# Kernel optimization log

Measured on AMD Instinct MI355X. Metric: run time of the kernel, lower is better.

## Reference

```python
import jax, jax.numpy as jnp
import numpy as np

B, T_ENC, VOCAB, HID = 256, 128, 1024, 1024
NUM_CLASSES = VOCAB - 1   # think_end_token
MAX_THINK = 16
N_OUT = T_ENC - 3


def setup_inputs() -> dict:
    key = jax.random.key(0)
    ks = jax.random.split(key, 8)
    s = 1.0 / np.sqrt(HID)
    x = jax.random.normal(ks[0], (B, T_ENC, VOCAB), jnp.float32)
    lengths = jax.random.randint(ks[1], (B,), 1, T_ENC + 1)  # valid lengths >= 1
    W_ih = jax.random.uniform(ks[2], (4 * HID, VOCAB), jnp.float32, -s, s)
    W_hh = jax.random.uniform(ks[3], (4 * HID, HID), jnp.float32, -s, s)
    b_ih = jax.random.uniform(ks[4], (4 * HID,), jnp.float32, -s, s)
    b_hh = jax.random.uniform(ks[5], (4 * HID,), jnp.float32, -s, s)
    W_fc = jax.random.uniform(ks[6], (VOCAB, HID), jnp.float32, -s, s)
    b_fc = jax.random.uniform(ks[7], (VOCAB,), jnp.float32, -s, s)
    return {"x": x, "W_ih": W_ih, "W_hh": W_hh, "b_ih": b_ih, "b_hh": b_hh,
            "W_fc": W_fc, "b_fc": b_fc, "lengths": lengths, "N": N_OUT}


def _lstm_cell(x_t, h, c, W_ih, W_hh, b):
    # torch gate order: i, f, g, o
    gates = x_t @ W_ih.T + h @ W_hh.T + b
    i, f, g, o = jnp.split(gates, 4, axis=-1)
    c_new = jax.nn.sigmoid(f) * c + jax.nn.sigmoid(i) * jnp.tanh(g)
    h_new = jax.nn.sigmoid(o) * jnp.tanh(c_new)
    return h_new, c_new


def reference(x, W_ih, W_hh, b_ih, b_hh, W_fc, b_fc, lengths, N):
    b = b_ih + b_hh
    Bsz = x.shape[0]
    h0 = jnp.zeros((Bsz, HID), x.dtype)
    c0 = jnp.zeros((Bsz, HID), x.dtype)

    # --- encoder: packed LSTM == masked scan, state frozen past each length ---
    def enc_step(carry, xt_t):
        h, c = carry
        xt, t = xt_t
        h_new, c_new = _lstm_cell(xt, h, c, W_ih, W_hh, b)
        m = (t < lengths)[:, None]
        return (jnp.where(m, h_new, h), jnp.where(m, c_new, c)), None

    (h, c), _ = jax.lax.scan(
        enc_step, (h0, c0),
        (jnp.transpose(x, (1, 0, 2)), jnp.arange(x.shape[1])))

    dec_in = x[jnp.arange(Bsz), lengths - 1, :]  # [B, VOCAB]
    T_dec = MAX_THINK + N  # while-loop terminates within this many steps
    fo0 = jnp.zeros((Bsz, N, VOCAB), x.dtype)
    key0 = jax.random.key(42)
    bidx = jnp.arange(Bsz)

    def dec_step(carry, t):
        h, c, cur, fo, think_steps, out_steps, is_think = carry
        outputting = (~is_think) & (out_steps < N)
        h, c = _lstm_cell(cur, h, c, W_ih, W_hh, b)
        logits = h @ W_fc.T + b_fc  # [B, VOCAB]
        # gumbel_softmax(tau=1, hard=True) with straight-through estimator
        gnoise = jax.random.gumbel(jax.random.fold_in(key0, t), logits.shape, logits.dtype)
        y_soft = jax.nn.softmax(logits + gnoise, axis=-1)
        y_hard = jax.nn.one_hot(jnp.argmax(y_soft, axis=-1), VOCAB, dtype=logits.dtype)
        one_hot_out = y_hard + y_soft - jax.lax.stop_gradient(y_soft)
        # masked scatter of logits into final_outputs at current output step
        step_idx = jnp.minimum(out_steps, N - 1)
        old = fo[bidx, step_idx]
        fo = fo.at[bidx, step_idx].set(jnp.where(outputting[:, None], logits, old))
        out_steps = out_steps + outputting.astype(out_steps.dtype)
        think_steps = think_steps + is_think.astype(think_steps.dtype)
        pred = jnp.argmax(one_hot_out, axis=-1)
        just_finished = is_think & ((pred == NUM_CLASSES) | (think_steps >= MAX_THINK))
        # original code: if any sample is thinking, next_input = logits for ALL
        nxt = jnp.where(jnp.any(is_think), logits, one_hot_out)
        is_think = is_think & (~just_finished)
        return (h, c, nxt, fo, think_steps, out_steps, is_think), None

    init = (h, c, dec_in, fo0,
            jnp.zeros(Bsz, jnp.int32), jnp.zeros(Bsz, jnp.int32),
            jnp.ones(Bsz, bool))
    (h, c, cur, fo, think_steps, out_steps, is_think), _ = jax.lax.scan(
        dec_step, init, jnp.arange(T_dec))
    return fo[:, :, :-1], think_steps
```

## Files before the change

kernel.cpp:

```cpp
#include <hip/hip_runtime.h>
#include <stdint.h>

#define HID 1024
#define NGATE 4096
#define BATCH 256
#define TENC 128
#define VOCAB 1024
#define NOUT 125
#define TDEC 141
#define MAXTHINK 16
#define STOPCLS 1023

typedef __attribute__((ext_vector_type(8))) short short8;
typedef __attribute__((ext_vector_type(4))) float f32x4;

#define WPLE ((size_t)NGATE*1024)
#define VPLE ((size_t)VOCAB*1024)
#define MFMA_B __builtin_amdgcn_mfma_f32_16x16x32_bf16

#define I_CLAIM 0
#define I_FLAGS 64
#define I_GEN   4224
#define I_ANY   4288
#define I_PRED  4608

#define LBAR() do { asm volatile("s_waitcnt lgkmcnt(0)" ::: "memory"); \
                    __builtin_amdgcn_s_barrier(); } while(0)

__device__ __forceinline__ uint32_t rotl32(uint32_t v, int r){ return (v<<r)|(v>>(32-r)); }

__device__ __forceinline__ void tf2x32(uint32_t k0, uint32_t k1, uint32_t x0, uint32_t x1,
                                       uint32_t& o0, uint32_t& o1)
{
  uint32_t k2 = k0 ^ k1 ^ 0x1BD11BDAu;
  x0 += k0; x1 += k1;
#define R4(a,b,cc,d) x0+=x1;x1=rotl32(x1,a);x1^=x0; x0+=x1;x1=rotl32(x1,b);x1^=x0; \
                     x0+=x1;x1=rotl32(x1,cc);x1^=x0; x0+=x1;x1=rotl32(x1,d);x1^=x0;
  R4(13,15,26,6)  x0+=k1; x1+=k2+1u;
  R4(17,29,16,24) x0+=k2; x1+=k0+2u;
  R4(13,15,26,6)  x0+=k0; x1+=k1+3u;
  R4(17,29,16,24) x0+=k1; x1+=k2+4u;
  R4(13,15,26,6)  x0+=k2; x1+=k0+5u;
#undef R4
  o0 = x0; o1 = x1;
}

__device__ __forceinline__ uint32_t jax_bits(uint32_t fk0, uint32_t fk1, uint32_t i)
{
  uint32_t o0, o1;
  tf2x32(fk0, fk1, 0u, i, o0, o1);
  return o0 ^ o1;
}

__device__ __forceinline__ float sigm(float x){ return 0.5f + 0.5f*tanhf(0.5f*x); }

__device__ __forceinline__ ushort bf16rn(float v){
  uint32_t u = __float_as_uint(v);
  uint32_t r = (u + 0x7fffu + ((u>>16)&1u)) >> 16;
  return (ushort)r;
}
__device__ __forceinline__ float bf16tof(ushort s){ return __uint_as_float(((uint32_t)s)<<16); }

typedef unsigned long long __attribute__((address_space(1))) gu64_t;
typedef int                __attribute__((address_space(1))) gi32_t;
typedef unsigned short     __attribute__((address_space(1))) gu16_t;

__device__ __forceinline__ uint64_t cld8(const ushort* p){
  return __hip_atomic_load((const gu64_t*)(uintptr_t)p, __ATOMIC_RELAXED, __HIP_MEMORY_SCOPE_AGENT);
}
__device__ __forceinline__ void cst8(ushort* p, uint64_t v){
  __hip_atomic_store((gu64_t*)(uintptr_t)p, v, __ATOMIC_RELAXED, __HIP_MEMORY_SCOPE_AGENT);
}
__device__ __forceinline__ float cld4f(const float* p){
  int v = __hip_atomic_load((const gi32_t*)(uintptr_t)p, __ATOMIC_RELAXED, __HIP_MEMORY_SCOPE_AGENT);
  return __int_as_float(v);
}
__device__ __forceinline__ void cst4f(float* p, float x){
  __hip_atomic_store((gi32_t*)(uintptr_t)p, __float_as_int(x), __ATOMIC_RELAXED, __HIP_MEMORY_SCOPE_AGENT);
}
__device__ __forceinline__ int cld4i(const int* p){
  return __hip_atomic_load((const gi32_t*)(uintptr_t)p, __ATOMIC_RELAXED, __HIP_MEMORY_SCOPE_AGENT);
}
__device__ __forceinline__ void cst4i(int* p, int v){
  __hip_atomic_store((gi32_t*)(uintptr_t)p, v, __ATOMIC_RELAXED, __HIP_MEMORY_SCOPE_AGENT);
}
__device__ __forceinline__ ushort cld2(const ushort* p){
  return __hip_atomic_load((const gu16_t*)(uintptr_t)p, __ATOMIC_RELAXED, __HIP_MEMORY_SCOPE_AGENT);
}
__device__ __forceinline__ void cst2(ushort* p, ushort v){
  __hip_atomic_store((gu16_t*)(uintptr_t)p, v, __ATOMIC_RELAXED, __HIP_MEMORY_SCOPE_AGENT);
}

typedef ushort GatesLds[2][3][32][40];
typedef ushort LdsXA[3][256][40];

__device__ __forceinline__ void gbar(int* flags, int* gen, int e, int rk, int tid)
{
  __syncthreads();
  if (tid == 0)
    __hip_atomic_store((gi32_t*)(uintptr_t)&flags[rk*16], e, __ATOMIC_RELAXED, __HIP_MEMORY_SCOPE_AGENT);
  if (rk == 0){
    if (tid < 256){
      while (cld4i(&flags[tid*16]) < e)
        __builtin_amdgcn_s_sleep(1);
    }
    __syncthreads();
    if (tid == 0)
      __hip_atomic_store((gi32_t*)(uintptr_t)gen, e, __ATOMIC_RELAXED, __HIP_MEMORY_SCOPE_AGENT);
  } else if (tid == 0){
    while (cld4i(gen) < e)
      __builtin_amdgcn_s_sleep(1);
  }
  __syncthreads();
}

__global__ __launch_bounds__(256) void prep_kernel(
    const float* __restrict__ b_ih, const float* __restrict__ b_hh,
    const float* __restrict__ x, const int* __restrict__ lengths,
    float* __restrict__ bsum, int* __restrict__ ints,
    ushort* __restrict__ h3i, ushort* __restrict__ cur3i,
    ushort* __restrict__ h3p0, ushort* __restrict__ curp0)
{
  int idx = blockIdx.x*256 + threadIdx.x;
  if (idx < NGATE) bsum[idx] = b_ih[idx] + b_hh[idx];
  if (idx < 8)   ints[I_CLAIM + idx] = 0;
  if (idx < 256) ints[I_FLAGS + idx*16] = 0;
  if (idx == 0)  ints[I_GEN] = 0;
  if (idx < TDEC+1) ints[I_ANY + idx] = (idx==0) ? 1 : 0;
  *(unsigned long long*)(h3i + (size_t)idx*4) = 0ull;
  h3p0[idx] = 0;
  int b = idx >> 10, k = idx & (HID-1);
  int L = lengths[b];
  float v = x[((size_t)b*TENC + (size_t)(L-1))*HID + k];
  ushort p0 = bf16rn(v); v -= bf16tof(p0);
  ushort p1 = bf16rn(v); v -= bf16tof(p1);
  ushort p2 = bf16rn(v);
  *(unsigned long long*)(cur3i + (size_t)idx*4) =
      (uint64_t)p0 | ((uint64_t)p1<<16) | ((uint64_t)p2<<32);
  curp0[idx] = p0;
}

__global__ __launch_bounds__(256) void splitw_kernel(
    const float* __restrict__ W, ushort* __restrict__ Wf, int N)
{
  int idx = blockIdx.x*256 + threadIdx.x;
  int n = idx >> 7, kc = idx & 127;
  float v[8];
  *(float4*)&v[0] = *(const float4*)(W + (size_t)n*1024 + kc*8);
  *(float4*)&v[4] = *(const float4*)(W + (size_t)n*1024 + kc*8 + 4);
  size_t base = ((size_t)(n>>4)*128 + kc)*128 + (n&15)*8;
  #pragma unroll
  for (int p=0;p<3;p++){
    ushort o[8];
    #pragma unroll
    for (int e=0;e<8;e++){ ushort pp = bf16rn(v[e]); v[e] -= bf16tof(pp); o[e] = pp; }
    *(uint4*)(Wf + (size_t)p*N*1024 + base) = *(uint4*)o;
  }
}


__device__ void xgemm_do(const float* __restrict__ x, const ushort* __restrict__ wih,
                         float* __restrict__ xg_x, int tc, int xcc, int rank,
                         char* xa_mem, int tid)
{
  LdsXA& xa = *reinterpret_cast<LdsXA*>(xa_mem);
  int lane = tid & 63, w = tid >> 6;
  int fr = lane & 15, q = lane >> 4;
  int tt = rank >> 2, g = rank & 3;
  int srow = tid >> 1, half = (tid & 1) * 16;
  const float* xrow = x + ((size_t)srow*TENC + (tc*8 + tt))*HID;
  size_t off = ((size_t)(g*64 + xcc*8 + w)*128 + q)*128 + fr*8;

#define LOADX(dst, kc) { \
  int kcl = ((kc) < 32) ? (kc) : 0; \
  _Pragma("unroll") for (int i=0;i<4;i++) \
    *(float4*)&dst[i*4] = *(const float4*)(xrow + kcl*32 + half + i*4); }

#define SPLITSTORE(xv) { \
  _Pragma("unroll") for (int p=0;p<3;p++){ \
    ushort o[16]; \
    _Pragma("unroll") for (int e=0;e<16;e++){ ushort pp = bf16rn(xv[e]); xv[e] -= bf16tof(pp); o[e] = pp; } \
    *(uint4*)&xa[p][srow][half]   = *(uint4*)&o[0]; \
    *(uint4*)&xa[p][srow][half+8] = *(uint4*)&o[8]; } }

#define XLOADB(dst, kc) { \
  int kcl = ((kc) < 32) ? (kc) : 0; \
  _Pragma("unroll") for (int p=0;p<3;p++) \
    dst[p] = *(const short8*)(wih + (size_t)p*WPLE + off + (size_t)kcl*512); }

#define XMFMA(bq) { \
  _Pragma("unroll") for (int mf=0; mf<16; mf++){ \
    short8 af[3]; \
    _Pragma("unroll") for (int p=0;p<3;p++) af[p] = *(const short8*)&xa[p][mf*16+fr][q*8]; \
    acc[mf] = MFMA_B(af[2], bq[0], acc[mf], 0,0,0); \
    acc[mf] = MFMA_B(af[1], bq[1], acc[mf], 0,0,0); \
    acc[mf] = MFMA_B(af[0], bq[2], acc[mf], 0,0,0); \
    acc[mf] = MFMA_B(af[1], bq[0], acc[mf], 0,0,0); \
    acc[mf] = MFMA_B(af[0], bq[1], acc[mf], 0,0,0); \
    acc[mf] = MFMA_B(af[0], bq[0], acc[mf], 0,0,0); } }

  f32x4 acc[16] = {};
  float xv0[16], xv1[16];
  short8 bq0[3], bq1[3];
  LOADX(xv0, 0); XLOADB(bq0, 0);
  for (int kc = 0; kc < 32; kc += 2){
    LBAR();
    SPLITSTORE(xv0);
    LBAR();
    LOADX(xv1, kc+1); XLOADB(bq1, kc+1);
    XMFMA(bq0);
    LBAR();
    SPLITSTORE(xv1);
    LBAR();
    LOADX(xv0, kc+2); XLOADB(bq0, kc+2);
    XMFMA(bq1);
  }
#undef LOADX
#undef SPLITSTORE
#undef XLOADB
#undef XMFMA
  #pragma unroll
  for (int mf=0; mf<16; mf++)
    #pragma unroll
    for (int r=0;r<4;r++)
      cst4f(xg_x + (size_t)(tt*256 + mf*16 + q*4 + r)*512 + g*128 + w*16 + fr, acc[mf][r]);
}

template<int PL, int MODE>
__device__ void gates_do(
    const ushort* __restrict__ A0i, const ushort* __restrict__ A1i,
    const ushort* __restrict__ A0c, const ushort* __restrict__ A1c,
    const ushort* __restrict__ Wih, const ushort* __restrict__ Whh,
    const float* __restrict__ Wihf, const int* __restrict__ pred,
    const float* __restrict__ xg_x,
    int t, const int* len2, const float (*bs2)[4],
    float* creg, ushort* __restrict__ h3newi, ushort* __restrict__ h3p0new,
    GatesLds& As, char* ep_mem,
    int xcc, int bb, int kg, int tid)
{
  constexpr int KT = (MODE==1) ? 64 : 32;
  float (*ep)[32][33] = reinterpret_cast<float(*)[32][33]>(ep_mem);
  int lane = tid & 63, w = tid >> 6;
  int fr = lane & 15, q = lane >> 4;
  int arow = tid >> 4, apos = tid & 15;
  int bf = w & 1, kf = (w>>1) & 1, gh = w >> 2;

  size_t off[2];
  #pragma unroll
  for (int g2=0; g2<2; g2++)
    off[g2] = ((size_t)((2*gh+g2)*64 + xcc*8 + kg*2 + kf)*128 + q)*128 + fr*8;

  f32x4 acc[2] = {};

#define LOADSA(sv, kc) { \
  int kcl = ((kc) < KT) ? (kc) : 0; \
  int kl = kcl & 31; \
  if constexpr (PL==3){ \
    const ushort* ai = (MODE==1 && kcl < 32) ? A0i : A1i; \
    _Pragma("unroll") for (int j=0;j<2;j++) \
      sv[j] = cld8(ai + ((size_t)(bb + arow)*1024 + kl*32 + apos*2 + j)*4); \
  } else { \
    const ushort* ac = (MODE==1 && kcl < 32) ? A0c : A1c; \
    sv[0] = (uint64_t)(uint)cld4i((const int*)(ac + (size_t)(bb + arow)*1024 + kl*32 + apos*2)); \
  } }

#define STAGE(buf, sv) { \
  if constexpr (PL==3){ \
    _Pragma("unroll") for (int p=0;p<3;p++){ \
      uint lo = (uint)((sv[0] >> (16*p)) & 0xffffu) | ((uint)((sv[1] >> (16*p)) & 0xffffu) << 16); \
      *(uint*)&As[buf][p][arow][apos*2] = lo; } \
  } else { \
    *(uint*)&As[buf][0][arow][apos*2] = (uint)sv[0]; \
  } }

#define LOADB(dst, kc) { \
  int kcl = ((kc) < KT) ? (kc) : 0; \
  const ushort* wsel = (MODE==1 && kcl < 32) ? Wih : Whh; \
  int kl = kcl & 31; \
  _Pragma("unroll") for (int p=0;p<PL;p++) \
  _Pragma("unroll") for (int g2=0; g2<2; g2++) \
    dst[p][g2] = *(const short8*)(wsel + (size_t)p*WPLE + off[g2] + (size_t)kl*512); }

#define READA(af, buf) { _Pragma("unroll") for (int p=0;p<PL;p++) af[p] = *(const short8*)&As[buf][p][bf*16 + fr][q*8]; }

#define DOMFMA(aa, bf_) { _Pragma("unroll") for (int g2=0; g2<2; g2++){ \
  if constexpr (PL==3){ \
    acc[g2] = MFMA_B(aa[2], bf_[0][g2], acc[g2], 0,0,0); \
    acc[g2] = MFMA_B(aa[1], bf_[1][g2], acc[g2], 0,0,0); \
    acc[g2] = MFMA_B(aa[0], bf_[2][g2], acc[g2], 0,0,0); \
    acc[g2] = MFMA_B(aa[1], bf_[0][g2], acc[g2], 0,0,0); \
    acc[g2] = MFMA_B(aa[0], bf_[1][g2], acc[g2], 0,0,0); \
    acc[g2] = MFMA_B(aa[0], bf_[0][g2], acc[g2], 0,0,0); \
  } else { \
    acc[g2] = MFMA_B(aa[0], bf_[0][g2], acc[g2], 0,0,0); \
  } } }

  uint64_t sv0[2], sv1[2], sv2[2], sv3[2];
  short8 bq0[PL][2], bq1[PL][2], afc[PL], afn[PL];
  LOADSA(sv0, 0); LOADSA(sv1, 1); LOADSA(sv2, 2); LOADSA(sv3, 3);
  LOADB(bq0, 0);
  STAGE(0, sv0); LBAR();
  READA(afc, 0);
  LOADSA(sv0, 4);
  for (int kc = 0; kc < KT; kc += 4){
    STAGE(1, sv1); LBAR();
    READA(afn, 1);
    LOADB(bq1, kc+1); LOADSA(sv1, kc+5);
    DOMFMA(afc, bq0);

    STAGE(0, sv2); LBAR();
    READA(afc, 0);
    LOADB(bq0, kc+2); LOADSA(sv2, kc+6);
    DOMFMA(afn, bq1);

    STAGE(1, sv3); LBAR();
    READA(afn, 1);
    LOADB(bq1, kc+3); LOADSA(sv3, kc+7);
    DOMFMA(afc, bq0);

    STAGE(0, sv0); LBAR();
    READA(afc, 0);
    LOADB(bq0, kc+4); LOADSA(sv0, kc+8);
    DOMFMA(afn, bq1);
  }
#undef LOADSA
#undef STAGE
#undef LOADB
#undef READA
#undef DOMFMA

  __syncthreads();
  #pragma unroll
  for (int g2=0; g2<2; g2++)
    #pragma unroll
    for (int r=0;r<4;r++)
      ep[2*gh+g2][bf*16 + q*4 + r][kf*16 + fr] = acc[g2][r];
  __syncthreads();

  #pragma unroll
  for (int e2=0; e2<2; e2++){
    int e = tid + e2*512;
    int b_loc = e >> 5, k_loc = e & 31;
    int b = bb + b_loc;
    int kkloc = kg*32 + k_loc;
    int kkg = xcc*128 + kkloc;
    size_t eidx = (size_t)b*1024 + kkg;
    if (MODE==0 && t >= len2[e2]){
      cst8(h3newi + eidx*4, cld8(A1i + eidx*4));
      cst2(h3p0new + eidx, cld2(A1c + eidx));
      continue;
    }
    float gi = ep[0][b_loc][k_loc], gf = ep[1][b_loc][k_loc];
    float gg2v = ep[2][b_loc][k_loc], go = ep[3][b_loc][k_loc];
    if (MODE==0){
      const float* xr = xg_x + (size_t)((t&7)*256 + b)*512;
      gi   += cld4f(xr + kkloc);
      gf   += cld4f(xr + 128 + kkloc);
      gg2v += cld4f(xr + 256 + kkloc);
      go   += cld4f(xr + 384 + kkloc);
    }
    if (MODE==2){
      int pp = cld4i(pred + b);
      gi   += Wihf[(size_t)(        kkg)*1024 + pp];
      gf   += Wihf[(size_t)(1024 + kkg)*1024 + pp];
      gg2v += Wihf[(size_t)(2048 + kkg)*1024 + pp];
      go   += Wihf[(size_t)(3072 + kkg)*1024 + pp];
    }
    gi += bs2[e2][0]; gf += bs2[e2][1]; gg2v += bs2[e2][2]; go += bs2[e2][3];
    float cn = sigm(gf)*creg[e2] + sigm(gi)*tanhf(gg2v);
    float hn = sigm(go)*tanhf(cn);
    creg[e2] = cn;
    float v = hn;
    ushort p0 = bf16rn(v); v -= bf16tof(p0);
    cst2(h3p0new + eidx, p0);
    if constexpr (PL==3){
      ushort p1 = bf16rn(v); v -= bf16tof(p1);
      ushort p2 = bf16rn(v);
      cst8(h3newi + eidx*4, (uint64_t)p0 | ((uint64_t)p1<<16) | ((uint64_t)p2<<32));
    }
  }
}

template<int PL>
__device__ void fc_do(
    const ushort* __restrict__ h3i, const ushort* __restrict__ h3c,
    const ushort* __restrict__ wfc,
    float* __restrict__ logits, GatesLds& As,
    int xcc, int bb, int vg, int tid)
{
  int lane = tid & 63, w = tid >> 6;
  int fr = lane & 15, q = lane >> 4;
  int arow = tid >> 4, apos = tid & 15;
  int bf = w & 1, vf = (w>>1) & 1;
  bool act = (w < 4);
  size_t off = ((size_t)(xcc*8 + vg*2 + vf)*128 + q)*128 + fr*8;
  f32x4 acc = {};

#define FLOADSA(sv, kc) { \
  int kcl = ((kc) < 32) ? (kc) : 0; \
  if constexpr (PL==3){ \
    _Pragma("unroll") for (int j=0;j<2;j++) \
      sv[j] = cld8(h3i + ((size_t)(bb + arow)*1024 + kcl*32 + apos*2 + j)*4); \
  } else { \
    sv[0] = (uint64_t)(uint)cld4i((const int*)(h3c + (size_t)(bb + arow)*1024 + kcl*32 + apos*2)); \
  } }

#define FSTAGE(buf, sv) { \
  if constexpr (PL==3){ \
    _Pragma("unroll") for (int p=0;p<3;p++){ \
      uint lo = (uint)((sv[0] >> (16*p)) & 0xffffu) | ((uint)((sv[1] >> (16*p)) & 0xffffu) << 16); \
      *(uint*)&As[buf][p][arow][apos*2] = lo; } \
  } else { \
    *(uint*)&As[buf][0][arow][apos*2] = (uint)sv[0]; \
  } }

#define FLOADB(dst, kc) { if (act){ \
  int kcl = ((kc) < 32) ? (kc) : 0; \
  _Pragma("unroll") for (int p=0;p<PL;p++) \
    dst[p] = *(const short8*)(wfc + (size_t)p*VPLE + off + (size_t)kcl*512); } }

#define FMM(aa, bf_) { if (act){ \
  if constexpr (PL==3){ \
    acc = MFMA_B(aa[2], bf_[0], acc, 0,0,0); \
    acc = MFMA_B(aa[1], bf_[1], acc, 0,0,0); \
    acc = MFMA_B(aa[0], bf_[2], acc, 0,0,0); \
    acc = MFMA_B(aa[1], bf_[0], acc, 0,0,0); \
    acc = MFMA_B(aa[0], bf_[1], acc, 0,0,0); \
    acc = MFMA_B(aa[0], bf_[0], acc, 0,0,0); \
  } else { \
    acc = MFMA_B(aa[0], bf_[0], acc, 0,0,0); \
  } } }

#define FREADA(af, buf) { if (act){ _Pragma("unroll") for (int p=0;p<PL;p++) af[p] = *(const short8*)&As[buf][p][bf*16 + fr][q*8]; } }

  uint64_t sv0[2], sv1[2], sv2[2], sv3[2];
  short8 bq0[PL], bq1[PL], afc[PL], afn[PL];
  FLOADSA(sv0, 0); FLOADSA(sv1, 1); FLOADSA(sv2, 2); FLOADSA(sv3, 3);
  FLOADB(bq0, 0);
  FSTAGE(0, sv0); LBAR();
  FREADA(afc, 0);
  FLOADSA(sv0, 4);
  for (int kc = 0; kc < 32; kc += 4){
    FSTAGE(1, sv1); LBAR();
    FREADA(afn, 1);
    FLOADB(bq1, kc+1); FLOADSA(sv1, kc+5);
    FMM(afc, bq0);

    FSTAGE(0, sv2); LBAR();
    FREADA(afc, 0);
    FLOADB(bq0, kc+2); FLOADSA(sv2, kc+6);
    FMM(afn, bq1);

    FSTAGE(1, sv3); LBAR();
    FREADA(afn, 1);
    FLOADB(bq1, kc+3); FLOADSA(sv3, kc+7);
    FMM(afc, bq0);

    FSTAGE(0, sv0); LBAR();
    FREADA(afc, 0);
    FLOADB(bq0, kc+4); FLOADSA(sv0, kc+8);
    FMM(afn, bq1);
  }
#undef FLOADSA
#undef FSTAGE
#undef FLOADB
#undef FMM
#undef FREADA

  if (act){
    int v = xcc*128 + vg*32 + vf*16 + fr;
    #pragma unroll
    for (int r=0;r<4;r++)
      cst4f(logits + (size_t)(bb + bf*16 + q*4 + r)*1024 + v, acc[r]);
  }
}

__device__ void decide_do(
    const float* __restrict__ logits, const float* __restrict__ b_fc, int t, int b,
    int* anyA, int* pred, float* __restrict__ out,
    ushort* __restrict__ cur3i, ushort* __restrict__ curp0,
    int& isth, int& tsteps, int& osteps,
    float* s_red, int* s_idx, int* s_misc, int tid)
{
  if (tid==0) s_misc[0] = cld4i(anyA + t);
  uint32_t fk0, fk1; tf2x32(0u, 42u, 0u, (uint32_t)t, fk0, fk1);
  float lg[2];
  float zb = -3.4e38f; int ib = 0;
  #pragma unroll
  for (int q2=0;q2<2;q2++){
    int v = tid + (q2<<9);
    uint32_t bits = jax_bits(fk0, fk1, (uint32_t)(b*VOCAB + v));
    float f = __uint_as_float((bits>>9) | 0x3F800000u) - 1.0f;
    const float TINY = 1.17549435e-38f;
    float u = fmaxf(TINY, f + TINY);
    float g = -logf(-logf(u));
    float l = cld4f(logits + (size_t)b*VOCAB + v) + b_fc[v];
    lg[q2] = l;
    float zz = l + g;
    if (zz > zb){ zb = zz; ib = v; }
  }
  s_red[tid] = zb; s_idx[tid] = ib;
  __syncthreads();
  for (int s2=256;s2>0;s2>>=1){
    if (tid < s2){
      float om = s_red[tid+s2]; int oi = s_idx[tid+s2];
      if (om > s_red[tid] || (om==s_red[tid] && oi < s_idx[tid])){ s_red[tid]=om; s_idx[tid]=oi; }
    }
    __syncthreads();
  }
  int predv = s_idx[0];
  int anyv  = s_misc[0];
  int outp = (!isth && osteps < NOUT) ? 1 : 0;
  int si = osteps < (NOUT-1) ? osteps : (NOUT-1);
  int nts = tsteps + (isth ? 1 : 0);
  int jf = (isth && ((predv==STOPCLS) || (nts >= MAXTHINK))) ? 1 : 0;
  int isnew = (isth && !jf) ? 1 : 0;
  if (tid==0){
    cst4i(pred + b, predv);
    if (isnew) __hip_atomic_fetch_or(&anyA[t+1], 1, __ATOMIC_RELAXED, __HIP_MEMORY_SCOPE_AGENT);
    if (t == TDEC-1) out[(size_t)BATCH*NOUT*(VOCAB-1) + b] = (float)nts;
  }
  osteps += outp; tsteps = nts; isth = isnew;
  #pragma unroll
  for (int q2=0;q2<2;q2++){
    int v = tid + (q2<<9);
    float l = lg[q2];
    float cv = anyv ? l : (v==predv ? 1.0f : 0.0f);
    if (t < MAXTHINK){
      float t2 = cv;
      ushort p0 = bf16rn(t2); t2 -= bf16tof(p0);
      ushort p1 = bf16rn(t2); t2 -= bf16tof(p1);
      ushort p2 = bf16rn(t2);
      cst8(cur3i + ((size_t)b*1024 + v)*4,
           (uint64_t)p0 | ((uint64_t)p1<<16) | ((uint64_t)p2<<32));
      cst2(curp0 + (size_t)b*1024 + v, p0);
    }
    if (outp && v < (VOCAB-1))
      out[((size_t)b*NOUT + si)*(VOCAB-1) + v] = l;
  }
}

struct KP {
  const float *x, *W_ih, *b_fc, *bsum;
  const int *lengths;
  float *logits, *out, *xg;
  ushort *h3a, *h3b, *cur3, *wih3, *whh3, *wfc3;
  ushort *h3p0a, *h3p0b, *curp0;
  int *ints;
  int guard;
};

__global__ __launch_bounds__(512, 2) void persist(KP P)
{
  __shared__ __align__(16) char xa_mem[61440];
  __shared__ __align__(16) GatesLds As;
  __shared__ float s_red[512];
  __shared__ int s_idx[512];
  __shared__ int s_misc[16];
  __shared__ char lds_pad[8192];
  if (P.guard) ((volatile char*)lds_pad)[0] = 1;

  int tid = threadIdx.x;
  int xcc; asm("s_getreg_b32 %0, hwreg(HW_REG_XCC_ID)" : "=s"(xcc));
  xcc &= 7;
  if (tid == 0)
    s_misc[8] = __hip_atomic_fetch_add(&P.ints[I_CLAIM + xcc], 1, __ATOMIC_RELAXED, __HIP_MEMORY_SCOPE_AGENT);
  __syncthreads();
  int rank  = s_misc[8] & 31;
  int rk256 = xcc*32 + rank;

  int bg = rank >> 2, kg = rank & 3;
  int bb = bg * 32;

  float bs2[2][4]; int len2[2]; float creg[2] = {0.f, 0.f};
  #pragma unroll
  for (int e2=0; e2<2; e2++){
    int e = tid + e2*512;
    int b_loc = e >> 5, k_loc = e & 31;
    int b = bb + b_loc;
    int kkg = xcc*128 + kg*32 + k_loc;
    #pragma unroll
    for (int g=0; g<4; g++) bs2[e2][g] = P.bsum[g*1024 + kkg];
    len2[e2] = P.lengths[b];
  }

  int* flags = P.ints + I_FLAGS;
  int* gen   = P.ints + I_GEN;
  int* anyA  = P.ints + I_ANY;
  int* pred  = P.ints + I_PRED;
  int epoch = 0;
  ushort* h3[2]   = { P.h3a,   P.h3b };
  ushort* h3p0[2] = { P.h3p0a, P.h3p0b };
  int hc = 0;
  int isth = 1, tsteps = 0, osteps = 0;
  float* xg_x = P.xg + (size_t)xcc*2048*512;

#define GBAR() gbar(flags, gen, ++epoch, rk256, tid)

  for (int tc = 0; tc < TENC/8; ++tc){
    xgemm_do(P.x, P.wih3, xg_x, tc, xcc, rank, xa_mem, tid);
    GBAR();
    for (int tt = 0; tt < 8; ++tt){
      int t = tc*8 + tt;
      gates_do<3,0>(nullptr, h3[hc], nullptr, h3p0[hc], nullptr, P.whh3, nullptr, nullptr, xg_x,
                    t, len2, bs2, creg, h3[hc^1], h3p0[hc^1], As, xa_mem, xcc, bb, kg, tid);
      hc ^= 1;
      GBAR();
    }
  }

  for (int t = 0; t < TDEC; ++t){
    if (t < MAXTHINK)
      gates_do<3,1>(P.cur3, h3[hc], nullptr, nullptr, P.wih3, P.whh3, nullptr, nullptr, nullptr,
                    t, len2, bs2, creg, h3[hc^1], h3p0[hc^1], As, xa_mem, xcc, bb, kg, tid);
    else if (t == MAXTHINK)
      gates_do<1,1>(nullptr, nullptr, P.curp0, h3p0[hc], P.wih3, P.whh3, nullptr, nullptr, nullptr,
                    t, len2, bs2, creg, h3[hc^1], h3p0[hc^1], As, xa_mem, xcc, bb, kg, tid);
    else
      gates_do<1,2>(nullptr, nullptr, nullptr, h3p0[hc], nullptr, P.whh3, P.W_ih, pred, nullptr,
                    t, len2, bs2, creg, h3[hc^1], h3p0[hc^1], As, xa_mem, xcc, bb, kg, tid);
    hc ^= 1;
    GBAR();
    if (t < MAXTHINK) fc_do<3>(h3[hc], nullptr, P.wfc3, P.logits, As, xcc, bb, kg, tid);
    else              fc_do<1>(nullptr, h3p0[hc], P.wfc3, P.logits, As, xcc, bb, kg, tid);
    GBAR();
    decide_do(P.logits, P.b_fc, t, rk256, anyA, pred, P.out, P.cur3, P.curp0,
              isth, tsteps, osteps, s_red, s_idx, s_misc, tid);
    GBAR();
  }
#undef GBAR
}

extern "C" void kernel_launch(void* const* d_in, const int* in_sizes, int n_in,
                              void* d_out, int out_size, void* d_ws, size_t ws_size,
                              hipStream_t stream)
{
  const float* x    = (const float*)d_in[0];
  const float* W_ih = (const float*)d_in[1];
  const float* W_hh = (const float*)d_in[2];
  const float* b_ih = (const float*)d_in[3];
  const float* b_hh = (const float*)d_in[4];
  const float* W_fc = (const float*)d_in[5];
  const float* b_fc = (const float*)d_in[6];
  const int*   lengths = (const int*)d_in[7];
  float* out = (float*)d_out;
  char* W = (char*)d_ws;

  constexpr size_t OF_BSUM = 0;
  constexpr size_t OF_LG   = OF_BSUM + 16384;
  constexpr size_t OF_H3A  = OF_LG   + 1048576;
  constexpr size_t OF_H3B  = OF_H3A  + 2097152;
  constexpr size_t OF_CUR3 = OF_H3B  + 2097152;
  constexpr size_t OF_P0A  = OF_CUR3 + 2097152;
  constexpr size_t OF_P0B  = OF_P0A  + 524288;
  constexpr size_t OF_CP0  = OF_P0B  + 524288;
  constexpr size_t OF_WIH  = OF_CP0  + 524288;
  constexpr size_t OF_WHH  = OF_WIH  + (size_t)3*NGATE*1024*2;
  constexpr size_t OF_WFC  = OF_WHH  + (size_t)3*NGATE*1024*2;
  constexpr size_t OF_INTS = OF_WFC  + (size_t)3*VOCAB*1024*2;

  float* bsum   = (float*)(W + OF_BSUM);
  float* logits = (float*)(W + OF_LG);
  ushort* h3a   = (ushort*)(W + OF_H3A);
  ushort* h3b   = (ushort*)(W + OF_H3B);
  ushort* cur3i = (ushort*)(W + OF_CUR3);
  ushort* h3p0a = (ushort*)(W + OF_P0A);
  ushort* h3p0b = (ushort*)(W + OF_P0B);
  ushort* curp0 = (ushort*)(W + OF_CP0);
  ushort* wih3  = (ushort*)(W + OF_WIH);
  ushort* whh3  = (ushort*)(W + OF_WHH);
  ushort* wfc3  = (ushort*)(W + OF_WFC);
  int* ints = (int*)(W + OF_INTS);

  float* xg = (float*)d_out;

  splitw_kernel<<<NGATE/2, 256, 0, stream>>>(W_ih, wih3, NGATE);
  splitw_kernel<<<NGATE/2, 256, 0, stream>>>(W_hh, whh3, NGATE);
  splitw_kernel<<<VOCAB/2, 256, 0, stream>>>(W_fc, wfc3, VOCAB);
  prep_kernel<<<1024, 256, 0, stream>>>(b_ih, b_hh, x, lengths, bsum, ints,
                                        h3a, cur3i, h3p0a, curp0);

  KP P;
  P.x = x; P.W_ih = W_ih; P.b_fc = b_fc; P.bsum = bsum; P.lengths = lengths;
  P.logits = logits; P.out = out; P.xg = xg;
  P.h3a = h3a; P.h3b = h3b; P.cur3 = cur3i;
  P.wih3 = wih3; P.whh3 = whh3; P.wfc3 = wfc3;
  P.h3p0a = h3p0a; P.h3p0b = h3p0b; P.curp0 = curp0;
  P.ints = ints;
  P.guard = 0;

  persist<<<dim3(256), dim3(512), 0, stream>>>(P);
}
```

Measured before the change: 8.883 ms.

## Fuse encoder input projection into per-step gate GEMM, dropping chunked xgemm

Removes the separate chunked x@W_ih GEMM that precomputed input gates for 8 timesteps into a global buffer. Each encoder step now runs a K=2048 gate GEMM: it loads x rows directly, splits them into three bf16 planes on the fly and concatenates them with h. This removes the xg global round-trip, the extra barrier per chunk and the 60KB LDS staging buffer. The cost is a serial step that is twice as deep, since the input projection now sits on the recurrent critical path instead of being batched across 8 steps.

```diff
diff --git a/kernel.cpp b/kernel.cpp
--- a/kernel.cpp
+++ b/kernel.cpp
@@ -92,7 +92,6 @@
 }
 
 typedef ushort GatesLds[2][3][32][40];
-typedef ushort LdsXA[3][256][40];
 
 __device__ __forceinline__ void gbar(int* flags, int* gen, int e, int rk, int tid)
 {
@@ -159,86 +158,19 @@
 }
 
 
-__device__ void xgemm_do(const float* __restrict__ x, const ushort* __restrict__ wih,
-                         float* __restrict__ xg_x, int tc, int xcc, int rank,
-                         char* xa_mem, int tid)
-{
-  LdsXA& xa = *reinterpret_cast<LdsXA*>(xa_mem);
-  int lane = tid & 63, w = tid >> 6;
-  int fr = lane & 15, q = lane >> 4;
-  int tt = rank >> 2, g = rank & 3;
-  int srow = tid >> 1, half = (tid & 1) * 16;
-  const float* xrow = x + ((size_t)srow*TENC + (tc*8 + tt))*HID;
-  size_t off = ((size_t)(g*64 + xcc*8 + w)*128 + q)*128 + fr*8;
-
-#define LOADX(dst, kc) { \
-  int kcl = ((kc) < 32) ? (kc) : 0; \
-  _Pragma("unroll") for (int i=0;i<4;i++) \
-    *(float4*)&dst[i*4] = *(const float4*)(xrow + kcl*32 + half + i*4); }
-
-#define SPLITSTORE(xv) { \
-  _Pragma("unroll") for (int p=0;p<3;p++){ \
-    ushort o[16]; \
-    _Pragma("unroll") for (int e=0;e<16;e++){ ushort pp = bf16rn(xv[e]); xv[e] -= bf16tof(pp); o[e] = pp; } \
-    *(uint4*)&xa[p][srow][half]   = *(uint4*)&o[0]; \
-    *(uint4*)&xa[p][srow][half+8] = *(uint4*)&o[8]; } }
-
-#define XLOADB(dst, kc) { \
-  int kcl = ((kc) < 32) ? (kc) : 0; \
-  _Pragma("unroll") for (int p=0;p<3;p++) \
-    dst[p] = *(const short8*)(wih + (size_t)p*WPLE + off + (size_t)kcl*512); }
-
-#define XMFMA(bq) { \
-  _Pragma("unroll") for (int mf=0; mf<16; mf++){ \
-    short8 af[3]; \
-    _Pragma("unroll") for (int p=0;p<3;p++) af[p] = *(const short8*)&xa[p][mf*16+fr][q*8]; \
-    acc[mf] = MFMA_B(af[2], bq[0], acc[mf], 0,0,0); \
-    acc[mf] = MFMA_B(af[1], bq[1], acc[mf], 0,0,0); \
-    acc[mf] = MFMA_B(af[0], bq[2], acc[mf], 0,0,0); \
-    acc[mf] = MFMA_B(af[1], bq[0], acc[mf], 0,0,0); \
-    acc[mf] = MFMA_B(af[0], bq[1], acc[mf], 0,0,0); \
-    acc[mf] = MFMA_B(af[0], bq[0], acc[mf], 0,0,0); } }
-
-  f32x4 acc[16] = {};
-  float xv0[16], xv1[16];
-  short8 bq0[3], bq1[3];
-  LOADX(xv0, 0); XLOADB(bq0, 0);
-  for (int kc = 0; kc < 32; kc += 2){
-    LBAR();
-    SPLITSTORE(xv0);
-    LBAR();
-    LOADX(xv1, kc+1); XLOADB(bq1, kc+1);
-    XMFMA(bq0);
-    LBAR();
-    SPLITSTORE(xv1);
-    LBAR();
-    LOADX(xv0, kc+2); XLOADB(bq0, kc+2);
-    XMFMA(bq1);
-  }
-#undef LOADX
-#undef SPLITSTORE
-#undef XLOADB
-#undef XMFMA
-  #pragma unroll
-  for (int mf=0; mf<16; mf++)
-    #pragma unroll
-    for (int r=0;r<4;r++)
-      cst4f(xg_x + (size_t)(tt*256 + mf*16 + q*4 + r)*512 + g*128 + w*16 + fr, acc[mf][r]);
-}
-
 template<int PL, int MODE>
 __device__ void gates_do(
     const ushort* __restrict__ A0i, const ushort* __restrict__ A1i,
     const ushort* __restrict__ A0c, const ushort* __restrict__ A1c,
     const ushort* __restrict__ Wih, const ushort* __restrict__ Whh,
     const float* __restrict__ Wihf, const int* __restrict__ pred,
-    const float* __restrict__ xg_x,
+    const float* __restrict__ xsrc,
     int t, const int* len2, const float (*bs2)[4],
     float* creg, ushort* __restrict__ h3newi, ushort* __restrict__ h3p0new,
     GatesLds& As, char* ep_mem,
     int xcc, int bb, int kg, int tid)
 {
-  constexpr int KT = (MODE==1) ? 64 : 32;
+  constexpr int KT = (MODE==2) ? 32 : 64;
   float (*ep)[32][33] = reinterpret_cast<float(*)[32][33]>(ep_mem);
   int lane = tid & 63, w = tid >> 6;
   int fr = lane & 15, q = lane >> 4;
@@ -256,9 +188,24 @@
   int kcl = ((kc) < KT) ? (kc) : 0; \
   int kl = kcl & 31; \
   if constexpr (PL==3){ \
-    const ushort* ai = (MODE==1 && kcl < 32) ? A0i : A1i; \
-    _Pragma("unroll") for (int j=0;j<2;j++) \
-      sv[j] = cld8(ai + ((size_t)(bb + arow)*1024 + kl*32 + apos*2 + j)*4); \
+    if (MODE==0 && kcl < 32){ \
+      const float* xp = xsrc + ((size_t)(bb + arow)*TENC + t)*HID + kl*32 + apos*2; \
+      float2 xv = *(const float2*)xp; \
+      float v0 = xv.x; \
+      ushort a0 = bf16rn(v0); v0 -= bf16tof(a0); \
+      ushort a1 = bf16rn(v0); v0 -= bf16tof(a1); \
+      ushort a2 = bf16rn(v0); \
+      float v1 = xv.y; \
+      ushort c0 = bf16rn(v1); v1 -= bf16tof(c0); \
+      ushort c1 = bf16rn(v1); v1 -= bf16tof(c1); \
+      ushort c2 = bf16rn(v1); \
+      sv[0] = (uint64_t)a0 | ((uint64_t)a1<<16) | ((uint64_t)a2<<32); \
+      sv[1] = (uint64_t)c0 | ((uint64_t)c1<<16) | ((uint64_t)c2<<32); \
+    } else { \
+      const ushort* ai = (MODE==1 && kcl < 32) ? A0i : A1i; \
+      _Pragma("unroll") for (int j=0;j<2;j++) \
+        sv[j] = cld8(ai + ((size_t)(bb + arow)*1024 + kl*32 + apos*2 + j)*4); \
+    } \
   } else { \
     const ushort* ac = (MODE==1 && kcl < 32) ? A0c : A1c; \
     sv[0] = (uint64_t)(uint)cld4i((const int*)(ac + (size_t)(bb + arow)*1024 + kl*32 + apos*2)); \
@@ -275,7 +222,7 @@
 
 #define LOADB(dst, kc) { \
   int kcl = ((kc) < KT) ? (kc) : 0; \
-  const ushort* wsel = (MODE==1 && kcl < 32) ? Wih : Whh; \
+  const ushort* wsel = (MODE!=2 && kcl < 32) ? Wih : Whh; \
   int kl = kcl & 31; \
   _Pragma("unroll") for (int p=0;p<PL;p++) \
   _Pragma("unroll") for (int g2=0; g2<2; g2++) \
@@ -352,13 +299,6 @@
     }
     float gi = ep[0][b_loc][k_loc], gf = ep[1][b_loc][k_loc];
     float gg2v = ep[2][b_loc][k_loc], go = ep[3][b_loc][k_loc];
-    if (MODE==0){
-      const float* xr = xg_x + (size_t)((t&7)*256 + b)*512;
-      gi   += cld4f(xr + kkloc);
-      gf   += cld4f(xr + 128 + kkloc);
-      gg2v += cld4f(xr + 256 + kkloc);
-      go   += cld4f(xr + 384 + kkloc);
-    }
     if (MODE==2){
       int pp = cld4i(pred + b);
       gi   += Wihf[(size_t)(        kkg)*1024 + pp];
@@ -543,7 +483,7 @@
 struct KP {
   const float *x, *W_ih, *b_fc, *bsum;
   const int *lengths;
-  float *logits, *out, *xg;
+  float *logits, *out;
   ushort *h3a, *h3b, *cur3, *wih3, *whh3, *wfc3;
   ushort *h3p0a, *h3p0b, *curp0;
   int *ints;
@@ -552,13 +492,13 @@
 
 __global__ __launch_bounds__(512, 2) void persist(KP P)
 {
-  __shared__ __align__(16) char xa_mem[61440];
+  __shared__ __align__(16) char ep_mem[17408];
   __shared__ __align__(16) GatesLds As;
   __shared__ float s_red[512];
   __shared__ int s_idx[512];
   __shared__ int s_misc[16];
-  __shared__ char lds_pad[8192];
-  if (P.guard) ((volatile char*)lds_pad)[0] = 1;
+  __shared__ char lds_pad[49152];
+  if (P.guard){ ((volatile char*)lds_pad)[0] = 1; ((volatile char*)ep_mem)[0] = 1; }
 
   int tid = threadIdx.x;
   int xcc; asm("s_getreg_b32 %0, hwreg(HW_REG_XCC_ID)" : "=s"(xcc));
@@ -593,32 +533,26 @@
   ushort* h3p0[2] = { P.h3p0a, P.h3p0b };
   int hc = 0;
   int isth = 1, tsteps = 0, osteps = 0;
-  float* xg_x = P.xg + (size_t)xcc*2048*512;
 
 #define GBAR() gbar(flags, gen, ++epoch, rk256, tid)
 
-  for (int tc = 0; tc < TENC/8; ++tc){
-    xgemm_do(P.x, P.wih3, xg_x, tc, xcc, rank, xa_mem, tid);
+  for (int t = 0; t < TENC; ++t){
+    gates_do<3,0>(nullptr, h3[hc], nullptr, h3p0[hc], P.wih3, P.whh3, nullptr, nullptr, P.x,
+                  t, len2, bs2, creg, h3[hc^1], h3p0[hc^1], As, ep_mem, xcc, bb, kg, tid);
+    hc ^= 1;
     GBAR();
-    for (int tt = 0; tt < 8; ++tt){
-      int t = tc*8 + tt;
-      gates_do<3,0>(nullptr, h3[hc], nullptr, h3p0[hc], nullptr, P.whh3, nullptr, nullptr, xg_x,
-                    t, len2, bs2, creg, h3[hc^1], h3p0[hc^1], As, xa_mem, xcc, bb, kg, tid);
-      hc ^= 1;
-      GBAR();
-    }
   }
 
   for (int t = 0; t < TDEC; ++t){
     if (t < MAXTHINK)
       gates_do<3,1>(P.cur3, h3[hc], nullptr, nullptr, P.wih3, P.whh3, nullptr, nullptr, nullptr,
-                    t, len2, bs2, creg, h3[hc^1], h3p0[hc^1], As, xa_mem, xcc, bb, kg, tid);
+                    t, len2, bs2, creg, h3[hc^1], h3p0[hc^1], As, ep_mem, xcc, bb, kg, tid);
     else if (t == MAXTHINK)
       gates_do<1,1>(nullptr, nullptr, P.curp0, h3p0[hc], P.wih3, P.whh3, nullptr, nullptr, nullptr,
-                    t, len2, bs2, creg, h3[hc^1], h3p0[hc^1], As, xa_mem, xcc, bb, kg, tid);
+                    t, len2, bs2, creg, h3[hc^1], h3p0[hc^1], As, ep_mem, xcc, bb, kg, tid);
     else
       gates_do<1,2>(nullptr, nullptr, nullptr, h3p0[hc], nullptr, P.whh3, P.W_ih, pred, nullptr,
-                    t, len2, bs2, creg, h3[hc^1], h3p0[hc^1], As, xa_mem, xcc, bb, kg, tid);
+                    t, len2, bs2, creg, h3[hc^1], h3p0[hc^1], As, ep_mem, xcc, bb, kg, tid);
     hc ^= 1;
     GBAR();
     if (t < MAXTHINK) fc_do<3>(h3[hc], nullptr, P.wfc3, P.logits, As, xcc, bb, kg, tid);
@@ -672,8 +606,6 @@
   ushort* wfc3  = (ushort*)(W + OF_WFC);
   int* ints = (int*)(W + OF_INTS);
 
-  float* xg = (float*)d_out;
-
   splitw_kernel<<<NGATE/2, 256, 0, stream>>>(W_ih, wih3, NGATE);
   splitw_kernel<<<NGATE/2, 256, 0, stream>>>(W_hh, whh3, NGATE);
   splitw_kernel<<<VOCAB/2, 256, 0, stream>>>(W_fc, wfc3, VOCAB);
@@ -682,7 +614,7 @@
 
   KP P;
   P.x = x; P.W_ih = W_ih; P.b_fc = b_fc; P.bsum = bsum; P.lengths = lengths;
-  P.logits = logits; P.out = out; P.xg = xg;
+  P.logits = logits; P.out = out;
   P.h3a = h3a; P.h3b = h3b; P.cur3 = cur3i;
   P.wih3 = wih3; P.whh3 = whh3; P.wfc3 = wfc3;
   P.h3p0a = h3p0a; P.h3p0b = h3p0b; P.curp0 = curp0;
```

Result: slower. 11.53 ms (+29.8%).
